# Performance work log

Hardware: AMD Instinct MI355X
Metric: run time of the kernel (lower is better)

Reference implementation:

```python
import jax, jax.numpy as jnp
import numpy as np

NUM_HEADS = 12
KEEP_RATE = 0.7
EPS = 1e-5  # torch nn.LayerNorm default


def layernorm(x, w, b):
    m = x.mean(-1, keepdims=True)
    v = ((x - m) ** 2).mean(-1, keepdims=True)
    return (x - m) * jax.lax.rsqrt(v + EPS) * w + b


def complement_idx(idx, dim):
    # idx: (B, L) top-k indices into [0, dim). Returns (B, dim-L) sorted complement,
    # matching EViT's scatter-zeros-then-sort trick.
    a = jnp.broadcast_to(jnp.arange(dim, dtype=idx.dtype), idx.shape[:-1] + (dim,))
    masked = jax.vmap(lambda ar, ix: ar.at[ix].set(0))(a, idx)
    n_idx = idx.shape[-1]
    return jnp.sort(masked, axis=-1)[..., n_idx:]


def setup_inputs() -> dict:
    key = jax.random.key(0)
    ks = jax.random.split(key, 8)
    B, N, C = 128, 197, 768
    H = 4 * C
    std = 0.02
    return {
        "x": jax.random.normal(ks[0], (B, N, C), jnp.float32),
        "norm1_w": jnp.ones((C,), jnp.float32),
        "norm1_b": jnp.zeros((C,), jnp.float32),
        "qkv_w": jax.random.normal(ks[1], (C, 3 * C), jnp.float32) * std,  # qkv_bias=False
        "proj_w": jax.random.normal(ks[2], (C, C), jnp.float32) * std,
        "proj_b": jnp.zeros((C,), jnp.float32),
        "norm2_w": jnp.ones((C,), jnp.float32),
        "norm2_b": jnp.zeros((C,), jnp.float32),
        "fc1_w": jax.random.normal(ks[3], (C, H), jnp.float32) * std,
        "fc1_b": jnp.zeros((H,), jnp.float32),
        "fc2_w": jax.random.normal(ks[4], (H, C), jnp.float32) * std,
        "fc2_b": jnp.zeros((C,), jnp.float32),
    }


def reference(x, norm1_w, norm1_b, qkv_w, proj_w, proj_b,
              norm2_w, norm2_b, fc1_w, fc1_b, fc2_w, fc2_b):
    B, N, C = x.shape
    h = NUM_HEADS
    d = C // h
    scale = d ** -0.5

    # ---- Attention (eval mode, no dropout) ----
    xn = layernorm(x, norm1_w, norm1_b)
    qkv = (xn @ qkv_w).reshape(B, N, 3, h, d).transpose(2, 0, 3, 1, 4)
    q, k, v = qkv[0], qkv[1], qkv[2]  # (B, h, N, d)
    attn = jax.nn.softmax(jnp.einsum('bhqd,bhkd->bhqk', q, k) * scale, axis=-1)
    out = jnp.einsum('bhqk,bhkd->bhqd', attn, v).transpose(0, 2, 1, 3).reshape(B, N, C)
    x = x + (out @ proj_w + proj_b)

    # ---- Top-k token selection (keep_rate < 1) ----
    left = int(np.ceil(KEEP_RATE * (N - 1)))          # 138 kept patch tokens
    cls_attn = attn[:, :, 0, 1:].mean(axis=1)         # (B, N-1)
    _, idx = jax.lax.top_k(cls_attn, left)            # sorted descending, like torch.topk
    compl = complement_idx(idx, N - 1)                # (B, M), M = N-1-left

    non_cls = x[:, 1:]                                # (B, N-1, C)
    gather = lambda arr, ix: jnp.take_along_axis(arr, ix[..., None], axis=1)

    x_others = gather(non_cls, idx)                   # (B, L, C)
    non_topk = gather(non_cls, compl)                 # (B, M, C)
    xo_n = x_others / jnp.linalg.norm(x_others, axis=-1, keepdims=True)
    nt_n = non_topk / jnp.linalg.norm(non_topk, axis=-1, keepdims=True)
    distance = jnp.einsum('bmc,blc->bml', nt_n, xo_n)  # cosine similarity (B, M, L)

    # attention-weighted merge of pruned tokens into nearest kept token
    non_cls_w = non_cls * cls_attn[..., None]
    x_others = gather(non_cls_w, idx)
    non_topk = gather(non_cls_w, compl)
    topk_attn = jnp.take_along_axis(cls_attn, idx, axis=1)       # (B, L)
    non_topk_attn = jnp.take_along_axis(cls_attn, compl, axis=1)  # (B, M)
    node_idx = jnp.argmax(distance, axis=-1)                      # (B, M)

    topk_attn = jax.vmap(lambda t, ni, nt: t.at[ni].add(nt))(topk_attn, node_idx, non_topk_attn)
    x_others = jax.vmap(lambda xo, ni, nt: xo.at[ni].add(nt))(x_others, node_idx, non_topk)
    x_others = x_others / topk_attn[..., None]

    x = jnp.concatenate([x[:, :1], x_others], axis=1)  # (B, L+1, C)

    # ---- MLP ----
    xn2 = layernorm(x, norm2_w, norm2_b)
    hmid = jax.nn.gelu(xn2 @ fc1_w + fc1_b, approximate=False)
    x = x + (hmid @ fc2_w + fc2_b)
    return x
```

## Files before the change

kernel.cpp:

```cpp
#include <hip/hip_runtime.h>
#include <math.h>

#define B_ 128
#define N_ 197
#define C_ 768
#define H_ 12
#define D_ 64
#define KEEP_ 138
#define COMP_ 58
#define NOUT_ 139
#define HID_ 3072

typedef __attribute__((ext_vector_type(8))) short bf16x8;
typedef __attribute__((ext_vector_type(8))) _Float16 f16x8;
typedef __attribute__((ext_vector_type(4))) float f32x4;
typedef unsigned short us;

__device__ inline us f2bf(float f) {
    unsigned u = __float_as_uint(f);
    unsigned r = (u + 0x7FFFu + ((u >> 16) & 1u)) >> 16;
    return (us)r;
}
__device__ inline float bf2f(us h) { return __uint_as_float(((unsigned)h) << 16); }
__device__ inline void gload_lds16(const void* g, void* l) {
    __builtin_amdgcn_global_load_lds((const __attribute__((address_space(1))) void*)g,
                                     (__attribute__((address_space(3))) void*)l, 16, 0, 0);
}
__device__ inline void split3(float v, us& h1, us& h2, us& h3) {
    h1 = f2bf(v);
    float r1 = v - bf2f(h1);
    h2 = f2bf(r1);
    h3 = f2bf(r1 - bf2f(h2));
}
__device__ inline void split2h(float v, us& h1, us& h2) {
    float av = fabsf(v);
    float v1 = (av < 6.103515625e-05f) ? 0.f : v;
    _Float16 a = (_Float16)v1;
    float r = (v - (float)a) * 4096.0f;
    _Float16 b = (_Float16)r;
    h1 = *reinterpret_cast<us*>(&a);
    h2 = *reinterpret_cast<us*>(&b);
}

__device__ inline float fast_gelu(float v) {
    float x = v * 0.70710678118654752f;
    float ax = fabsf(x);
    float t = __frcp_rn(__fmaf_rn(0.3275911f, ax, 1.0f));
    float p = __fmaf_rn(1.061405429f, t, -1.453152027f);
    p = __fmaf_rn(p, t, 1.421413741f);
    p = __fmaf_rn(p, t, -0.284496736f);
    p = __fmaf_rn(p, t, 0.254829592f);
    p = p * t;
    float e = __expf(-x * x);
    float erfa = __fmaf_rn(-p, e, 1.0f);
    float er = (x < 0.f) ? -erfa : erfa;
    return 0.5f * v * (1.0f + er);
}

__device__ inline void xcd_swizzle(int GX, int GY, int& bx, int& by) {
    int nwg = GX * GY;
    int orig = by * GX + bx;
    int q = nwg >> 3, r = nwg & 7;
    int xcd = orig & 7, idx = orig >> 3;
    int wgid = (xcd < r ? xcd * (q + 1) : r * (q + 1) + (xcd - r) * q) + idx;
    bx = wgid % GX;
    by = wgid / GX;
}

#define WAITV(n) asm volatile("s_waitcnt vmcnt(" #n ")" ::: "memory")
#define RBAR __builtin_amdgcn_s_barrier()

__global__ __launch_bounds__(256) void ln_split2h_kernel(const float* __restrict__ x,
                                                         const float* __restrict__ w,
                                                         const float* __restrict__ bias,
                                                         us* __restrict__ y1,
                                                         us* __restrict__ y2) {
    int row = blockIdx.x;
    const float* xr = x + (size_t)row * C_;
    int tid = threadIdx.x;
    float v[3];
    float s = 0.f, sq = 0.f;
#pragma unroll
    for (int i = 0; i < 3; i++) {
        v[i] = xr[tid + i * 256];
        s += v[i];
        sq += v[i] * v[i];
    }
    __shared__ float s1[256], s2[256];
    s1[tid] = s; s2[tid] = sq;
    __syncthreads();
    for (int o = 128; o > 0; o >>= 1) {
        if (tid < o) { s1[tid] += s1[tid + o]; s2[tid] += s2[tid + o]; }
        __syncthreads();
    }
    float mean = s1[0] * (1.0f / C_);
    float var = s2[0] * (1.0f / C_) - mean * mean;
    float rstd = rsqrtf(var + 1e-5f);
#pragma unroll
    for (int i = 0; i < 3; i++) {
        int c = tid + i * 256;
        float y = (v[i] - mean) * rstd * w[c] + bias[c];
        us h1, h2;
        split2h(y, h1, h2);
        size_t o = (size_t)row * C_ + c;
        y1[o] = h1; y2[o] = h2;
    }
}

__global__ __launch_bounds__(256) void ln2bf_kernel(const float* __restrict__ x,
                                                    const float* __restrict__ w,
                                                    const float* __restrict__ bias,
                                                    us* __restrict__ y) {
    int row = blockIdx.x;
    const float* xr = x + (size_t)row * C_;
    us* yr = y + (size_t)row * C_;
    int tid = threadIdx.x;
    float v[3];
    float s = 0.f, sq = 0.f;
#pragma unroll
    for (int i = 0; i < 3; i++) {
        v[i] = xr[tid + i * 256];
        s += v[i];
        sq += v[i] * v[i];
    }
    __shared__ float s1[256], s2[256];
    s1[tid] = s; s2[tid] = sq;
    __syncthreads();
    for (int o = 128; o > 0; o >>= 1) {
        if (tid < o) { s1[tid] += s1[tid + o]; s2[tid] += s2[tid + o]; }
        __syncthreads();
    }
    float mean = s1[0] * (1.0f / C_);
    float var = s2[0] * (1.0f / C_) - mean * mean;
    float rstd = rsqrtf(var + 1e-5f);
#pragma unroll
    for (int i = 0; i < 3; i++) {
        int c = tid + i * 256;
        yr[c] = f2bf((v[i] - mean) * rstd * w[c] + bias[c]);
    }
}

__global__ __launch_bounds__(256) void wtrans_kernel(const float* __restrict__ in,
                                                     us* __restrict__ out,
                                                     int K, int N) {
    __shared__ float T[32][33];
    int n0 = blockIdx.x * 32, k0 = blockIdx.y * 32;
    int tx = threadIdx.x & 31, ty = threadIdx.x >> 5;
    for (int i = 0; i < 32; i += 8)
        T[ty + i][tx] = in[(size_t)(k0 + ty + i) * N + n0 + tx];
    __syncthreads();
    for (int i = 0; i < 32; i += 8)
        out[(size_t)(n0 + ty + i) * K + k0 + tx] = f2bf(T[tx][ty + i]);
}

__global__ __launch_bounds__(256) void wtrans_split2h_kernel(const float* __restrict__ in,
                                                             us* __restrict__ o1,
                                                             us* __restrict__ o2,
                                                             int K, int N) {
    __shared__ float T[32][33];
    int n0 = blockIdx.x * 32, k0 = blockIdx.y * 32;
    int tx = threadIdx.x & 31, ty = threadIdx.x >> 5;
    for (int i = 0; i < 32; i += 8)
        T[ty + i][tx] = in[(size_t)(k0 + ty + i) * N + n0 + tx];
    __syncthreads();
    for (int i = 0; i < 32; i += 8) {
        us h1, h2;
        split2h(T[tx][ty + i], h1, h2);
        size_t o = (size_t)(n0 + ty + i) * K + k0 + tx;
        o1[o] = h1; o2[o] = h2;
    }
}

template <bool BIAS, bool RES>
__global__ __launch_bounds__(256, 2) void bgemm3h_kernel(const us* __restrict__ A1,
                                                         const us* __restrict__ A2,
                                                         const us* __restrict__ B1,
                                                         const us* __restrict__ B2,
                                                         const float* __restrict__ bias,
                                                         const float* __restrict__ res,
                                                         float* __restrict__ Cm,
                                                         int M, int N, int K) {
    __shared__ short As[2][128 * 64];
    __shared__ short Bs[2][128 * 64];
    int tid = threadIdx.x;
    int lane = tid & 63, wid = tid >> 6;
    int wr = wid >> 1, wc = wid & 1;
    int lr = lane & 15, g = lane >> 4;
    int bx = blockIdx.x, by = blockIdx.y;
    xcd_swizzle(gridDim.x, gridDim.y, bx, by);
    int brow = by * 128, bcol = bx * 128;

    f32x4 acc0[4][4] = {};
    f32x4 acc1[4][4] = {};

    for (int k0 = 0; k0 < K; k0 += 64) {
#pragma unroll
        for (int v = 0; v < 4; v++) {
            int rowb = v * 32 + wid * 8;
            int r = rowb + (lane >> 3);
            int slot = lane & 7;
            int chunk = slot ^ (r & 7);
            int garow = brow + r; if (garow >= M) garow = M - 1;
            int gbrow = bcol + r;
            gload_lds16(A1 + (size_t)garow * K + k0 + chunk * 8, &As[0][rowb * 64]);
            gload_lds16(A2 + (size_t)garow * K + k0 + chunk * 8, &As[1][rowb * 64]);
            gload_lds16(B1 + (size_t)gbrow * K + k0 + chunk * 8, &Bs[0][rowb * 64]);
            gload_lds16(B2 + (size_t)gbrow * K + k0 + chunk * 8, &Bs[1][rowb * 64]);
        }
        __syncthreads();
#pragma unroll
        for (int kk = 0; kk < 2; kk++) {
            f16x8 af[2][4], bfr[2][4];
#pragma unroll
            for (int fi = 0; fi < 4; fi++) {
                int ra = wr * 64 + fi * 16 + lr;
                int sla = (kk * 4 + g) ^ (ra & 7);
                int rb = wc * 64 + fi * 16 + lr;
                int slb = (kk * 4 + g) ^ (rb & 7);
#pragma unroll
                for (int s = 0; s < 2; s++) {
                    af[s][fi] = *reinterpret_cast<const f16x8*>(&As[s][ra * 64 + sla * 8]);
                    bfr[s][fi] = *reinterpret_cast<const f16x8*>(&Bs[s][rb * 64 + slb * 8]);
                }
            }
#pragma unroll
            for (int fi = 0; fi < 4; fi++)
#pragma unroll
                for (int fj = 0; fj < 4; fj++) {
                    acc0[fi][fj] = __builtin_amdgcn_mfma_f32_16x16x32_f16(af[0][fi], bfr[0][fj], acc0[fi][fj], 0, 0, 0);
                    acc1[fi][fj] = __builtin_amdgcn_mfma_f32_16x16x32_f16(af[0][fi], bfr[1][fj], acc1[fi][fj], 0, 0, 0);
                    acc1[fi][fj] = __builtin_amdgcn_mfma_f32_16x16x32_f16(af[1][fi], bfr[0][fj], acc1[fi][fj], 0, 0, 0);
                }
        }
        __syncthreads();
    }
#pragma unroll
    for (int fi = 0; fi < 4; fi++) {
#pragma unroll
        for (int fj = 0; fj < 4; fj++) {
            int col = bcol + wc * 64 + fj * 16 + lr;
            float bv = BIAS ? bias[col] : 0.f;
#pragma unroll
            for (int i = 0; i < 4; i++) {
                int r = brow + wr * 64 + fi * 16 + g * 4 + i;
                if (r < M) {
                    float vv = acc0[fi][fj][i] + acc1[fi][fj][i] * (1.0f / 4096.0f) + bv;
                    if (RES) vv += res[(size_t)r * N + col];
                    Cm[(size_t)r * N + col] = vv;
                }
            }
        }
    }
}

template <bool GELU_, bool OUTBF, bool RES>
__global__ __launch_bounds__(256, 4) void bgemm_kernel(const us* __restrict__ A,
                                                       const us* __restrict__ Bt,
                                                       const float* __restrict__ bias,
                                                       const float* __restrict__ res,
                                                       void* __restrict__ Cout,
                                                       int M, int N, int K) {
    __shared__ short As[128 * 64];
    __shared__ short Bs[128 * 64];
    int tid = threadIdx.x;
    int lane = tid & 63, wid = tid >> 6;
    int wr = wid >> 1, wc = wid & 1;
    int lr = lane & 15, g = lane >> 4;
    int bx = blockIdx.x, by = blockIdx.y;
    xcd_swizzle(gridDim.x, gridDim.y, bx, by);
    int brow = by * 128, bcol = bx * 128;

    f32x4 acc[4][4] = {};

    for (int k0 = 0; k0 < K; k0 += 64) {
#pragma unroll
        for (int v = 0; v < 4; v++) {
            int rowb = v * 32 + wid * 8;
            int r = rowb + (lane >> 3);
            int slot = lane & 7;
            int chunk = slot ^ (r & 7);
            int garow = brow + r; if (garow >= M) garow = M - 1;
            gload_lds16(A + (size_t)garow * K + k0 + chunk * 8, &As[rowb * 64]);
            gload_lds16(Bt + (size_t)(bcol + r) * K + k0 + chunk * 8, &Bs[rowb * 64]);
        }
        __syncthreads();
#pragma unroll
        for (int kk = 0; kk < 2; kk++) {
            bf16x8 af[4], bfr[4];
#pragma unroll
            for (int fi = 0; fi < 4; fi++) {
                int ra = wr * 64 + fi * 16 + lr;
                int sla = (kk * 4 + g) ^ (ra & 7);
                int rb = wc * 64 + fi * 16 + lr;
                int slb = (kk * 4 + g) ^ (rb & 7);
                af[fi] = *reinterpret_cast<const bf16x8*>(&As[ra * 64 + sla * 8]);
                bfr[fi] = *reinterpret_cast<const bf16x8*>(&Bs[rb * 64 + slb * 8]);
            }
#pragma unroll
            for (int fi = 0; fi < 4; fi++)
#pragma unroll
                for (int fj = 0; fj < 4; fj++)
                    acc[fi][fj] = __builtin_amdgcn_mfma_f32_16x16x32_bf16(af[fi], bfr[fj], acc[fi][fj], 0, 0, 0);
        }
        __syncthreads();
    }
#pragma unroll
    for (int fi = 0; fi < 4; fi++) {
#pragma unroll
        for (int fj = 0; fj < 4; fj++) {
            int col = bcol + wc * 64 + fj * 16 + lr;
            float bv = bias[col];
#pragma unroll
            for (int i = 0; i < 4; i++) {
                int r = brow + wr * 64 + fi * 16 + g * 4 + i;
                if (r < M) {
                    float vv = acc[fi][fj][i] + bv;
                    if (GELU_) vv = fast_gelu(vv);
                    if (OUTBF) {
                        ((us*)Cout)[(size_t)r * N + col] = f2bf(vv);
                    } else {
                        if (RES) vv += res[(size_t)r * N + col];
                        ((float*)Cout)[(size_t)r * N + col] = vv;
                    }
                }
            }
        }
    }
}

__global__ __launch_bounds__(512, 1) void attn12_kernel(const float* __restrict__ qkv,
                                                        us* __restrict__ ao1,
                                                        us* __restrict__ ao2,
                                                        float* __restrict__ attn0,
                                                        int b0) {
    int hh = blockIdx.x, b = blockIdx.y;
    int tid = threadIdx.x, lane = tid & 63, wv = tid >> 6;
    int lr = lane & 15, g = lane >> 4;
    __shared__ short Ks[2][208 * 64];
    __shared__ short Vt[2][64 * 224];
    __shared__ unsigned Pscr[8][16 * 36];
    const size_t base = (size_t)b * N_ * 3 * C_ + (size_t)hh * D_;

    for (int i = tid; i < 208 * 8; i += 512) {
        int k = i >> 3, oct = i & 7;
        int d0 = (oct ^ (k & 7)) * 8;
        float tv[8];
        if (k < N_) {
            const float4* kp = reinterpret_cast<const float4*>(qkv + base + (size_t)k * 3 * C_ + C_ + d0);
            float4 aa = kp[0], bb = kp[1];
            tv[0] = aa.x; tv[1] = aa.y; tv[2] = aa.z; tv[3] = aa.w;
            tv[4] = bb.x; tv[5] = bb.y; tv[6] = bb.z; tv[7] = bb.w;
        } else {
#pragma unroll
            for (int e = 0; e < 8; e++) tv[e] = 0.f;
        }
        bf16x8 h1v, h2v;
#pragma unroll
        for (int e = 0; e < 8; e++) {
            us ha, hb;
            split2h(tv[e], ha, hb);
            h1v[e] = (short)ha; h2v[e] = (short)hb;
        }
        int di = k * 64 + oct * 8;
        *reinterpret_cast<bf16x8*>(&Ks[0][di]) = h1v;
        *reinterpret_cast<bf16x8*>(&Ks[1][di]) = h2v;
    }
    {
        int d = tid & 63, jb = tid >> 6;
        for (int it = 0; it < 28; it++) {
            int k = it * 8 + jb;
            float vv = (k < N_) ? qkv[base + (size_t)k * 3 * C_ + 2 * C_ + d] : 0.f;
            us p1 = f2bf(vv);
            us p2 = f2bf(vv - bf2f(p1));
            int idx = d * 224 + (((k >> 3) ^ (d & 3)) * 8) + (k & 7);
            Vt[0][idx] = (short)p1;
            Vt[1][idx] = (short)p2;
        }
    }
    __syncthreads();

#pragma unroll
    for (int chunk = 0; chunk < 2; chunk++) {
        int qbase = chunk * 128 + wv * 16;
        f16x8 qf1[2], qf2[2];
        int qrow = qbase + lr;
#pragma unroll
        for (int kk = 0; kk < 2; kk++) {
            float qv[8];
            if (qrow < N_) {
                const float4* qp = reinterpret_cast<const float4*>(qkv + base + (size_t)qrow * 3 * C_ + kk * 32 + g * 8);
                float4 aa = qp[0], bb = qp[1];
                qv[0] = aa.x; qv[1] = aa.y; qv[2] = aa.z; qv[3] = aa.w;
                qv[4] = bb.x; qv[5] = bb.y; qv[6] = bb.z; qv[7] = bb.w;
            } else {
#pragma unroll
                for (int e = 0; e < 8; e++) qv[e] = 0.f;
            }
#pragma unroll
            for (int e = 0; e < 8; e++) {
                us ha, hb;
                split2h(qv[e], ha, hb);
                qf1[kk][e] = *reinterpret_cast<_Float16*>(&ha);
                qf2[kk][e] = *reinterpret_cast<_Float16*>(&hb);
            }
        }
        f32x4 sacc[13] = {};
        f32x4 sacc1[13] = {};
#pragma unroll
        for (int kt = 0; kt < 13; kt++) {
#pragma unroll
            for (int kk = 0; kk < 2; kk++) {
                int row = kt * 16 + lr;
                int sl = ((kk * 4 + g) ^ (row & 7)) * 8;
                const f16x8 b1 = *reinterpret_cast<const f16x8*>(&Ks[0][row * 64 + sl]);
                const f16x8 b2 = *reinterpret_cast<const f16x8*>(&Ks[1][row * 64 + sl]);
                sacc[kt]  = __builtin_amdgcn_mfma_f32_16x16x32_f16(qf1[kk], b1, sacc[kt], 0, 0, 0);
                sacc1[kt] = __builtin_amdgcn_mfma_f32_16x16x32_f16(qf1[kk], b2, sacc1[kt], 0, 0, 0);
                sacc1[kt] = __builtin_amdgcn_mfma_f32_16x16x32_f16(qf2[kk], b1, sacc1[kt], 0, 0, 0);
            }
        }
#pragma unroll
        for (int kt = 0; kt < 13; kt++)
#pragma unroll
            for (int i = 0; i < 4; i++)
                sacc[kt][i] += sacc1[kt][i] * (1.0f / 4096.0f);
#pragma unroll
        for (int i = 0; i < 4; i++) {
            float m = -1e30f;
#pragma unroll
            for (int kt = 0; kt < 13; kt++) {
                int k = kt * 16 + lr;
                float lgv = (k < N_) ? sacc[kt][i] * 0.125f : -1e30f;
                sacc[kt][i] = lgv;
                m = fmaxf(m, lgv);
            }
            m = fmaxf(m, __shfl_xor(m, 1, 64));
            m = fmaxf(m, __shfl_xor(m, 2, 64));
            m = fmaxf(m, __shfl_xor(m, 4, 64));
            m = fmaxf(m, __shfl_xor(m, 8, 64));
            float se = 0.f;
#pragma unroll
            for (int kt = 0; kt < 13; kt++) {
                int k = kt * 16 + lr;
                float e = (k < N_) ? expf(sacc[kt][i] - m) : 0.f;
                sacc[kt][i] = e;
                se += e;
            }
            se += __shfl_xor(se, 1, 64);
            se += __shfl_xor(se, 2, 64);
            se += __shfl_xor(se, 4, 64);
            se += __shfl_xor(se, 8, 64);
            float inv = 1.0f / se;
#pragma unroll
            for (int kt = 0; kt < 13; kt++) sacc[kt][i] *= inv;
        }
        if (chunk == 0 && wv == 0 && g == 0) {
#pragma unroll
            for (int kt = 0; kt < 13; kt++) {
                int k = kt * 16 + lr;
                if (k < N_) attn0[((size_t)(b0 + b) * H_ + hh) * N_ + k] = sacc[kt][0];
            }
        }
        f32x4 oacc[4] = {};
#pragma unroll
        for (int sect = 0; sect < 7; sect++) {
#pragma unroll
            for (int t = 0; t < 2; t++) {
                int kt = sect * 2 + t;
#pragma unroll
                for (int i = 0; i < 4; i++) {
                    float p = (kt < 13) ? sacc[kt][i] : 0.f;
                    us h1 = f2bf(p);
                    us h2 = f2bf(p - bf2f(h1));
                    Pscr[wv][(g * 4 + i) * 36 + t * 16 + lr] = (unsigned)h1 | ((unsigned)h2 << 16);
                }
            }
            uint4 u0 = *reinterpret_cast<const uint4*>(&Pscr[wv][lr * 36 + g * 8]);
            uint4 u1 = *reinterpret_cast<const uint4*>(&Pscr[wv][lr * 36 + g * 8 + 4]);
            unsigned uu[8] = {u0.x, u0.y, u0.z, u0.w, u1.x, u1.y, u1.z, u1.w};
            bf16x8 pa1, pa2;
#pragma unroll
            for (int e = 0; e < 8; e++) {
                pa1[e] = (short)(uu[e] & 0xffffu);
                pa2[e] = (short)(uu[e] >> 16);
            }
#pragma unroll
            for (int dt = 0; dt < 4; dt++) {
                int row = dt * 16 + lr;
                int cc = sect * 4 + g;
                int idx = row * 224 + ((cc ^ (row & 3)) * 8);
                const bf16x8 v1 = *reinterpret_cast<const bf16x8*>(&Vt[0][idx]);
                const bf16x8 v2 = *reinterpret_cast<const bf16x8*>(&Vt[1][idx]);
                oacc[dt] = __builtin_amdgcn_mfma_f32_16x16x32_bf16(pa1, v1, oacc[dt], 0, 0, 0);
                oacc[dt] = __builtin_amdgcn_mfma_f32_16x16x32_bf16(pa1, v2, oacc[dt], 0, 0, 0);
                oacc[dt] = __builtin_amdgcn_mfma_f32_16x16x32_bf16(pa2, v1, oacc[dt], 0, 0, 0);
            }
        }
#pragma unroll
        for (int dt = 0; dt < 4; dt++) {
#pragma unroll
            for (int i = 0; i < 4; i++) {
                int q = qbase + g * 4 + i;
                if (q < N_) {
                    int d = dt * 16 + lr;
                    size_t oi = ((size_t)(b * N_ + q)) * C_ + (size_t)hh * D_ + d;
                    us h1, h2;
                    split2h(oacc[dt][i], h1, h2);
                    ao1[oi] = h1; ao2[oi] = h2;
                }
            }
        }
    }
}

__global__ __launch_bounds__(256) void cls_kernel(const float* __restrict__ attn0,
                                                  float* __restrict__ cls) {
    int b = blockIdx.x, tid = threadIdx.x;
    if (tid < N_ - 1) {
        float s = 0.f;
        for (int hh = 0; hh < H_; hh++) s += attn0[((size_t)b * H_ + hh) * N_ + 1 + tid];
        cls[b * (N_ - 1) + tid] = s * (1.0f / H_);
    }
}

__global__ __launch_bounds__(256) void topk_kernel(const float* __restrict__ cls,
                                                   int* __restrict__ idx,
                                                   int* __restrict__ cmp) {
    int b = blockIdx.x, tid = threadIdx.x;
    __shared__ float vals[196];
    __shared__ int rk[196];
    if (tid < 196) vals[tid] = cls[b * 196 + tid];
    __syncthreads();
    if (tid < 196) {
        float v = vals[tid];
        int r = 0;
        for (int j = 0; j < 196; j++) {
            float u = vals[j];
            r += (u > v) || (u == v && j < tid);
        }
        rk[tid] = r;
    }
    __syncthreads();
    if (tid < 196) {
        int r = rk[tid];
        if (r < KEEP_) {
            idx[b * KEEP_ + r] = tid;
        } else {
            int pos = 0;
            for (int j = 0; j < tid; j++) pos += (rk[j] >= KEEP_);
            cmp[b * COMP_ + pos] = tid;
        }
    }
}

__global__ __launch_bounds__(256) void rnorm_kernel(const float* __restrict__ x1,
                                                    float* __restrict__ rn) {
    int i = blockIdx.x, b = blockIdx.y, tid = threadIdx.x;
    const float* xr = x1 + ((size_t)b * N_ + 1 + i) * C_;
    float sq = 0.f;
#pragma unroll
    for (int k = 0; k < 3; k++) {
        float v = xr[tid + k * 256];
        sq += v * v;
    }
    __shared__ float s2[256];
    s2[tid] = sq;
    __syncthreads();
    for (int o = 128; o > 0; o >>= 1) {
        if (tid < o) s2[tid] += s2[tid + o];
        __syncthreads();
    }
    if (tid == 0) rn[b * 196 + i] = rsqrtf(s2[0]);
}

__global__ __launch_bounds__(256, 3) void dist4_kernel(const float* __restrict__ x1,
                                                       const float* __restrict__ rn,
                                                       const int* __restrict__ idx,
                                                       const int* __restrict__ cmp,
                                                       int* __restrict__ node) {
    int b = blockIdx.x, half = blockIdx.y;
    int l0 = half * 29;
    int tid = threadIdx.x;
    __shared__ __align__(16) float As2[32][64];
    __shared__ __align__(16) float Bs2[138][64];
    __shared__ int cpl[29];
    __shared__ int til[KEEP_];
    __shared__ float rnt[KEEP_];
    if (tid < 29) cpl[tid] = cmp[b * COMP_ + l0 + tid];
    if (tid < KEEP_) {
        int t = idx[b * KEEP_ + tid];
        til[tid] = t;
        rnt[tid] = rn[b * 196 + t];
    }
    __syncthreads();
    int tr = tid >> 5, tc = tid & 31;
    int mb[5], mm[5];
#pragma unroll
    for (int j = 0; j < 5; j++) {
        int m = tc * 5 + j;
        int mc = (m < KEEP_) ? m : (KEEP_ - 1);
        mb[j] = mc * 64;
        mm[j] = mc & 15;
    }
    float acc[4][5] = {};
    for (int k0 = 0; k0 < C_; k0 += 64) {
        for (int ii = tid; ii < 29 * 16; ii += 256) {
            int l = ii >> 4, kc = ii & 15;
            *reinterpret_cast<float4*>(&As2[l][kc * 4]) =
                *reinterpret_cast<const float4*>(&x1[((size_t)b * N_ + 1 + cpl[l]) * C_ + k0 + kc * 4]);
        }
        for (int ii = tid; ii < KEEP_ * 16; ii += 256) {
            int m = ii >> 4, kc = ii & 15;
            *reinterpret_cast<float4*>(&Bs2[m][(kc ^ (m & 15)) * 4]) =
                *reinterpret_cast<const float4*>(&x1[((size_t)b * N_ + 1 + til[m]) * C_ + k0 + kc * 4]);
        }
        __syncthreads();
#pragma unroll 4
        for (int kc = 0; kc < 16; kc++) {
            float4 a4[4], b4[5];
#pragma unroll
            for (int i = 0; i < 4; i++)
                a4[i] = *reinterpret_cast<const float4*>(&As2[tr * 4 + i][kc * 4]);
#pragma unroll
            for (int j = 0; j < 5; j++)
                b4[j] = *reinterpret_cast<const float4*>(&Bs2[0][0] + mb[j] + ((kc ^ mm[j]) << 2));
#pragma unroll
            for (int i = 0; i < 4; i++)
#pragma unroll
                for (int j = 0; j < 5; j++) {
                    acc[i][j] += a4[i].x * b4[j].x;
                    acc[i][j] += a4[i].y * b4[j].y;
                    acc[i][j] += a4[i].z * b4[j].z;
                    acc[i][j] += a4[i].w * b4[j].w;
                }
        }
        __syncthreads();
    }
#pragma unroll
    for (int i = 0; i < 4; i++) {
        int ll = tr * 4 + i;
        if (ll < 29) {
            float best = -3.0e38f;
            int bm = 0x7fffffff;
#pragma unroll
            for (int j = 0; j < 5; j++) {
                int m = tc * 5 + j;
                if (m < KEEP_) {
                    float dv = acc[i][j] * rnt[m];
                    if (dv > best) { best = dv; bm = m; }
                }
            }
            for (int o = 1; o < 32; o <<= 1) {
                float ov = __shfl_xor(best, o, 64);
                int oi = __shfl_xor(bm, o, 64);
                if (ov > best || (ov == best && oi < bm)) { best = ov; bm = oi; }
            }
            if (tc == 0) node[b * COMP_ + l0 + ll] = bm;
        }
    }
}

__global__ __launch_bounds__(256) void fuse_kernel(const float* __restrict__ x1,
                                                   const float* __restrict__ cls,
                                                   const int* __restrict__ idx,
                                                   const int* __restrict__ cmp,
                                                   const int* __restrict__ node,
                                                   float* __restrict__ x2) {
    int mr = blockIdx.x, b = blockIdx.y, tid = threadIdx.x;
    if (mr == 0) {
        for (int c = tid; c < C_; c += 256)
            x2[(size_t)b * NOUT_ * C_ + c] = x1[(size_t)b * N_ * C_ + c];
        return;
    }
    int m = mr - 1;
    __shared__ int nds[COMP_];
    __shared__ int cps[COMP_];
    if (tid < COMP_) {
        nds[tid] = node[b * COMP_ + tid];
        cps[tid] = cmp[b * COMP_ + tid];
    }
    __syncthreads();
    int ti = idx[b * KEEP_ + m];
    float ta = cls[b * 196 + ti];
    float denom = ta;
    for (int l = 0; l < COMP_; l++)
        if (nds[l] == m) denom += cls[b * 196 + cps[l]];
    float a[3];
    const float* xr = x1 + ((size_t)b * N_ + 1 + ti) * C_;
#pragma unroll
    for (int i = 0; i < 3; i++) a[i] = xr[tid + i * 256] * ta;
    for (int l = 0; l < COMP_; l++) {
        if (nds[l] == m) {
            float ca = cls[b * 196 + cps[l]];
            const float* yr = x1 + ((size_t)b * N_ + 1 + cps[l]) * C_;
#pragma unroll
            for (int i = 0; i < 3; i++) a[i] += yr[tid + i * 256] * ca;
        }
    }
    float invd = 1.0f / denom;
#pragma unroll
    for (int i = 0; i < 3; i++)
        x2[((size_t)b * NOUT_ + mr) * C_ + tid + i * 256] = a[i] * invd;
}

extern "C" void kernel_launch(void* const* d_in, const int* in_sizes, int n_in,
                              void* d_out, int out_size, void* d_ws, size_t ws_size,
                              hipStream_t stream) {
    const float* x       = (const float*)d_in[0];
    const float* norm1_w = (const float*)d_in[1];
    const float* norm1_b = (const float*)d_in[2];
    const float* qkv_w   = (const float*)d_in[3];
    const float* proj_w  = (const float*)d_in[4];
    const float* proj_b  = (const float*)d_in[5];
    const float* norm2_w = (const float*)d_in[6];
    const float* norm2_b = (const float*)d_in[7];
    const float* fc1_w   = (const float*)d_in[8];
    const float* fc1_b   = (const float*)d_in[9];
    const float* fc2_w   = (const float*)d_in[10];
    const float* fc2_b   = (const float*)d_in[11];
    float* out = (float*)d_out;

    const int M1 = B_ * N_;
    const int M2 = B_ * NOUT_;
    const size_t WT_F  = 2359296;
    const size_t C3C   = (size_t)C_ * 3 * C_;
    const size_t CC    = (size_t)C_ * C_;

    const size_t small_f = (size_t)B_ * H_ * N_ + 2u * B_ * 196;
    const size_t small_i = (size_t)B_ * KEEP_ + 2u * B_ * COMP_;
    const size_t x1_f = (size_t)M1 * C_;

    const int cb_t[4] = {64, 32, 16, 4};
    const int rm_t[4] = {M2, M2, 4864, 320};
    int CB = 4, RMLP = 320;
    size_t scr_f = 0;
    {
        bool ok = false;
        for (int tier = 0; tier < 4; tier++) {
            int cb = cb_t[tier], rm = rm_t[tier];
            size_t cbnc = (size_t)cb * N_ * C_;
            size_t front_f = (C3C + CC) + cbnc + 3 * cbnc;
            size_t mlp_f   = WT_F + (size_t)rm * 1920;
            size_t sf      = front_f > mlp_f ? front_f : mlp_f;
            size_t nd      = (x1_f + sf + small_f) * 4 + small_i * 4;
            if (ws_size >= nd) { CB = cb; RMLP = rm; scr_f = sf; ok = true; break; }
        }
        if (!ok) return;
    }

    float* ws = (float*)d_ws;
    float* x1    = ws;
    float* scr   = x1 + x1_f;
    float* attn0 = scr + scr_f;
    float* cls   = attn0 + (size_t)B_ * H_ * N_;
    float* rn    = cls + B_ * 196;
    int* idxb    = (int*)(rn + B_ * 196);
    int* cmpb    = idxb + B_ * KEEP_;
    int* nodeb   = cmpb + B_ * COMP_;
    float* x2    = out;

    const size_t cbnc = (size_t)CB * N_ * C_;
    us* sb  = (us*)scr;
    us* qw1 = sb;            us* qw2 = qw1 + C3C;
    us* pw1 = qw2 + C3C;     us* pw2 = pw1 + CC;
    us* xn1 = pw2 + CC;      us* xn2 = xn1 + cbnc;
    float* qkv_c = (float*)(xn2 + cbnc);
    us* ao1 = xn1;  us* ao2 = xn2;
    us* fc1wt  = (us*)scr;
    us* fc2wt  = fc1wt + (size_t)C_ * HID_;
    us* xn2bf  = fc2wt + (size_t)C_ * HID_;
    us* hmidbf = xn2bf + (size_t)RMLP * C_;

    wtrans_split2h_kernel<<<dim3(3 * C_ / 32, C_ / 32), 256, 0, stream>>>(qkv_w, qw1, qw2, C_, 3 * C_);
    wtrans_split2h_kernel<<<dim3(C_ / 32, C_ / 32), 256, 0, stream>>>(proj_w, pw1, pw2, C_, C_);

    for (int b0 = 0; b0 < B_; b0 += CB) {
        int cb = (B_ - b0 < CB) ? (B_ - b0) : CB;
        int Mc = cb * N_;
        const float* xch = x + (size_t)b0 * N_ * C_;
        ln_split2h_kernel<<<Mc, 256, 0, stream>>>(xch, norm1_w, norm1_b, xn1, xn2);
        bgemm3h_kernel<false, false><<<dim3(3 * C_ / 128, (Mc + 127) / 128), 256, 0, stream>>>(
            xn1, xn2, qw1, qw2, nullptr, nullptr, qkv_c, Mc, 3 * C_, C_);
        attn12_kernel<<<dim3(H_, cb), 512, 0, stream>>>(qkv_c, ao1, ao2, attn0, b0);
        bgemm3h_kernel<true, true><<<dim3(C_ / 128, (Mc + 127) / 128), 256, 0, stream>>>(
            ao1, ao2, pw1, pw2, proj_b, xch, x1 + (size_t)b0 * N_ * C_, Mc, C_, C_);
    }

    cls_kernel<<<B_, 256, 0, stream>>>(attn0, cls);
    topk_kernel<<<B_, 256, 0, stream>>>(cls, idxb, cmpb);
    rnorm_kernel<<<dim3(196, B_), 256, 0, stream>>>(x1, rn);
    dist4_kernel<<<dim3(B_, 2), 256, 0, stream>>>(x1, rn, idxb, cmpb, nodeb);
    fuse_kernel<<<dim3(NOUT_, B_), 256, 0, stream>>>(x1, cls, idxb, cmpb, nodeb, x2);

    wtrans_kernel<<<dim3(HID_ / 32, C_ / 32), 256, 0, stream>>>(fc1_w, fc1wt, C_, HID_);
    wtrans_kernel<<<dim3(C_ / 32, HID_ / 32), 256, 0, stream>>>(fc2_w, fc2wt, HID_, C_);

    for (int r0 = 0; r0 < M2; r0 += RMLP) {
        int R = M2 - r0 < RMLP ? M2 - r0 : RMLP;
        ln2bf_kernel<<<R, 256, 0, stream>>>(x2 + (size_t)r0 * C_, norm2_w, norm2_b, xn2bf);
        bgemm_kernel<true, true, false><<<dim3(HID_ / 128, (R + 127) / 128), 256, 0, stream>>>(
            xn2bf, fc1wt, fc1_b, nullptr, hmidbf, R, HID_, C_);
        bgemm_kernel<false, false, true><<<dim3(C_ / 128, (R + 127) / 128), 256, 0, stream>>>(
            hmidbf, fc2wt, fc2_b, x2 + (size_t)r0 * C_, out + (size_t)r0 * C_, R, C_, HID_);
    }
}
```

Before: 1.302 ms.

## Enlarge MLP GEMM tiles to 256x256 with double-buffered LDS prefetch

```diff
diff --git a/kernel.cpp b/kernel.cpp
--- a/kernel.cpp
+++ b/kernel.cpp
@@ -254,65 +254,80 @@
 }
 
 template <bool GELU_, bool OUTBF, bool RES>
-__global__ __launch_bounds__(256, 4) void bgemm_kernel(const us* __restrict__ A,
+__global__ __launch_bounds__(512, 2) void bgemm_kernel(const us* __restrict__ A,
                                                        const us* __restrict__ Bt,
                                                        const float* __restrict__ bias,
                                                        const float* __restrict__ res,
                                                        void* __restrict__ Cout,
                                                        int M, int N, int K) {
-    __shared__ short As[128 * 64];
-    __shared__ short Bs[128 * 64];
+    __shared__ short As[2][256 * 64];
+    __shared__ short Bs[2][256 * 64];
     int tid = threadIdx.x;
     int lane = tid & 63, wid = tid >> 6;
-    int wr = wid >> 1, wc = wid & 1;
+    int wr = wid >> 2, wc = wid & 3;
     int lr = lane & 15, g = lane >> 4;
     int bx = blockIdx.x, by = blockIdx.y;
     xcd_swizzle(gridDim.x, gridDim.y, bx, by);
-    int brow = by * 128, bcol = bx * 128;
-
-    f32x4 acc[4][4] = {};
-
+    int brow = by * 256, bcol = bx * 256;
+
+    f32x4 acc[8][4] = {};
+
+    auto stage = [&](int buf, int k0) {
+#pragma unroll
+        for (int v = 0; v < 4; v++) {
+            int rowb = v * 64 + wid * 8;
+            int r = rowb + (lane >> 3);
+            int chunk = (lane & 7) ^ (r & 7);
+            int garow = brow + r; if (garow >= M) garow = M - 1;
+            gload_lds16(A + (size_t)garow * K + k0 + chunk * 8, &As[buf][rowb * 64]);
+            gload_lds16(Bt + (size_t)(bcol + r) * K + k0 + chunk * 8, &Bs[buf][rowb * 64]);
+        }
+    };
+    auto compute = [&](int buf) {
+#pragma unroll
+        for (int kk = 0; kk < 2; kk++) {
+            bf16x8 bfr[4];
+#pragma unroll
+            for (int fj = 0; fj < 4; fj++) {
+                int rb = wc * 64 + fj * 16 + lr;
+                int slb = (kk * 4 + g) ^ (rb & 7);
+                bfr[fj] = *reinterpret_cast<const bf16x8*>(&Bs[buf][rb * 64 + slb * 8]);
+            }
+#pragma unroll
+            for (int fi = 0; fi < 8; fi++) {
+                int ra = wr * 128 + fi * 16 + lr;
+                int sla = (kk * 4 + g) ^ (ra & 7);
+                bf16x8 af = *reinterpret_cast<const bf16x8*>(&As[buf][ra * 64 + sla * 8]);
+#pragma unroll
+                for (int fj = 0; fj < 4; fj++)
+                    acc[fi][fj] = __builtin_amdgcn_mfma_f32_16x16x32_bf16(af, bfr[fj], acc[fi][fj], 0, 0, 0);
+            }
+        }
+    };
+
+    stage(0, 0);
+    int cur = 0;
     for (int k0 = 0; k0 < K; k0 += 64) {
-#pragma unroll
-        for (int v = 0; v < 4; v++) {
-            int rowb = v * 32 + wid * 8;
-            int r = rowb + (lane >> 3);
-            int slot = lane & 7;
-            int chunk = slot ^ (r & 7);
-            int garow = brow + r; if (garow >= M) garow = M - 1;
-            gload_lds16(A + (size_t)garow * K + k0 + chunk * 8, &As[rowb * 64]);
-            gload_lds16(Bt + (size_t)(bcol + r) * K + k0 + chunk * 8, &Bs[rowb * 64]);
-        }
-        __syncthreads();
-#pragma unroll
-        for (int kk = 0; kk < 2; kk++) {
-            bf16x8 af[4], bfr[4];
-#pragma unroll
-            for (int fi = 0; fi < 4; fi++) {
-                int ra = wr * 64 + fi * 16 + lr;
-                int sla = (kk * 4 + g) ^ (ra & 7);
-                int rb = wc * 64 + fi * 16 + lr;
-                int slb = (kk * 4 + g) ^ (rb & 7);
-                af[fi] = *reinterpret_cast<const bf16x8*>(&As[ra * 64 + sla * 8]);
-                bfr[fi] = *reinterpret_cast<const bf16x8*>(&Bs[rb * 64 + slb * 8]);
-            }
-#pragma unroll
-            for (int fi = 0; fi < 4; fi++)
-#pragma unroll
-                for (int fj = 0; fj < 4; fj++)
-                    acc[fi][fj] = __builtin_amdgcn_mfma_f32_16x16x32_bf16(af[fi], bfr[fj], acc[fi][fj], 0, 0, 0);
-        }
-        __syncthreads();
-    }
-#pragma unroll
-    for (int fi = 0; fi < 4; fi++) {
+        if (k0 + 64 < K) {
+            stage(cur ^ 1, k0 + 64);
+            WAITV(8);
+        } else {
+            WAITV(0);
+        }
+        RBAR;
+        compute(cur);
+        RBAR;
+        cur ^= 1;
+    }
+#pragma unroll
+    for (int fi = 0; fi < 8; fi++) {
 #pragma unroll
         for (int fj = 0; fj < 4; fj++) {
             int col = bcol + wc * 64 + fj * 16 + lr;
             float bv = bias[col];
 #pragma unroll
             for (int i = 0; i < 4; i++) {
-                int r = brow + wr * 64 + fi * 16 + g * 4 + i;
+                int r = brow + wr * 128 + fi * 16 + g * 4 + i;
                 if (r < M) {
                     float vv = acc[fi][fj][i] + bv;
                     if (GELU_) vv = fast_gelu(vv);
@@ -798,9 +813,9 @@
     for (int r0 = 0; r0 < M2; r0 += RMLP) {
         int R = M2 - r0 < RMLP ? M2 - r0 : RMLP;
         ln2bf_kernel<<<R, 256, 0, stream>>>(x2 + (size_t)r0 * C_, norm2_w, norm2_b, xn2bf);
-        bgemm_kernel<true, true, false><<<dim3(HID_ / 128, (R + 127) / 128), 256, 0, stream>>>(
+        bgemm_kernel<true, true, false><<<dim3(HID_ / 256, (R + 255) / 256), 512, 0, stream>>>(
             xn2bf, fc1wt, fc1_b, nullptr, hmidbf, R, HID_, C_);
-        bgemm_kernel<false, false, true><<<dim3(C_ / 128, (R + 127) / 128), 256, 0, stream>>>(
+        bgemm_kernel<false, false, true><<<dim3(C_ / 256, (R + 255) / 256), 512, 0, stream>>>(
             hmidbf, fc2wt, fc2_b, x2 + (size_t)r0 * C_, out + (size_t)r0 * C_, R, C_, HID_);
     }
 }
```

After: 1.440 ms. 10.6% more time.
